# Optimization experiments

Hardware: AMD Instinct MI355X
Metric: run time of the kernel (lower is better)

The kernel has to match this reference:

```python
import jax, jax.numpy as jnp
import numpy as np

L2 = 65536          # edges per orientation (L=256 torus)
N = 2 * L2          # total edges
FIN = 8             # nfeatCNN_in
FOUT = 8            # nfeatCNN_out
K = 13              # kernel size (neighbor shifts per edge)
SCALE = (2.0 + 2.0 * np.e) / (np.e - 1.0)


def setup_inputs() -> dict:
    key = jax.random.key(0)
    ks = jax.random.split(key, 8)
    x = jax.random.normal(ks[0], (FIN * N,), dtype=jnp.float32)
    Wconv_hor = jax.random.normal(ks[1], (FOUT, FIN, K), dtype=jnp.float32) * 0.1
    Wconv_vert = jax.random.normal(ks[2], (FOUT, FIN, K), dtype=jnp.float32) * 0.1
    bconv_hor = jnp.zeros((FOUT,), dtype=jnp.float32)
    bconv_vert = jnp.zeros((FOUT,), dtype=jnp.float32)
    mask_hor = jax.random.randint(ks[3], (L2, FOUT, FIN, K), 0, 2).astype(bool)
    mask_vert = jax.random.randint(ks[4], (L2, FOUT, FIN, K), 0, 2).astype(bool)
    ker_hor = jax.random.randint(ks[5], (L2, K), 0, N, dtype=jnp.int32)
    ker_vert = jax.random.randint(ks[6], (L2, K), 0, N, dtype=jnp.int32)
    hor_edge_lst = jnp.arange(L2, dtype=jnp.int32)
    vert_edge_lst = jnp.arange(L2, dtype=jnp.int32) + L2
    return {
        "x": x,
        "Wconv_hor": Wconv_hor, "Wconv_vert": Wconv_vert,
        "bconv_hor": bconv_hor, "bconv_vert": bconv_vert,
        "mask_hor": mask_hor, "mask_vert": mask_vert,
        "ker_hor": ker_hor, "ker_vert": ker_vert,
        "hor_edge_lst": hor_edge_lst, "vert_edge_lst": vert_edge_lst,
    }


def reference(x, Wconv_hor, Wconv_vert, bconv_hor, bconv_vert,
              mask_hor, mask_vert, ker_hor, ker_vert,
              hor_edge_lst, vert_edge_lst):
    fout, fin, _ = Wconv_hor.shape
    n = x.shape[0] // fin
    xm = x.reshape(fin, n)                      # (fin, N)

    def branch(W, mask, ker, b):
        xg = xm[:, ker]                         # gather -> (fin, E, K)
        Wm = W[None] * mask.astype(W.dtype)     # (E, fout, fin, K)
        # per-edge masked contraction over (fin, K); vectorized over edges
        z = jnp.einsum('eoik,iek->oe', Wm, xg)  # (fout, E)
        return z + b[:, None]

    x_hor = branch(Wconv_hor, mask_hor, ker_hor, bconv_hor)
    x_vert = branch(Wconv_vert, mask_vert, ker_vert, bconv_vert)

    out = jnp.zeros((fout, n), dtype=x.dtype)
    out = out.at[:, hor_edge_lst].set(x_hor)
    out = out.at[:, vert_edge_lst].set(x_vert)
    return (jax.nn.sigmoid(out) - 0.5) * jnp.asarray(SCALE, out.dtype)
```

## Files before the change

kernel.cpp:

```cpp
#include <hip/hip_runtime.h>
#include <math.h>

#define L2C   65536
#define NC    (2 * L2C)
#define FINC  8
#define FOUTC 8
#define KC    13
#define BLOCK 256
#define EPB   4

constexpr double E_D = 2.71828182845904523536;
constexpr float SCALE_F = (float)((2.0 + 2.0 * E_D) / (E_D - 1.0));


__global__ __launch_bounds__(256)
void detect_mask_kernel(const unsigned char* __restrict__ m, int* __restrict__ flag) {
    __shared__ int any_nz;
    if (threadIdx.x == 0) any_nz = 0;
    __syncthreads();
    int local = 0;
    for (int e = threadIdx.x; e < 4096; e += 256) local |= m[(size_t)e * 4 + 1];
    if (local) atomicOr(&any_nz, 1);
    __syncthreads();
    if (threadIdx.x == 0) flag[0] = (any_nz == 0) ? 1 : 0;
}

__global__ __launch_bounds__(256)
void transpose_x_kernel(const float* __restrict__ x, float* __restrict__ xt) {
    int n = blockIdx.x * 256 + threadIdx.x;
    float v[FINC];
#pragma unroll
    for (int i = 0; i < FINC; ++i) v[i] = x[(size_t)i * NC + n];
    float4* dst = reinterpret_cast<float4*>(xt + ((size_t)n << 3));
    dst[0] = make_float4(v[0], v[1], v[2], v[3]);
    dst[1] = make_float4(v[4], v[5], v[6], v[7]);
}

__global__ __launch_bounds__(BLOCK)
void edge_conv_kernel(const float* __restrict__ xt,
                      const int* __restrict__ flag_p,
                      const float* __restrict__ Wh, const float* __restrict__ Wv,
                      const float* __restrict__ bh, const float* __restrict__ bv,
                      const unsigned char* __restrict__ mh,
                      const unsigned char* __restrict__ mv,
                      const int* __restrict__ kh, const int* __restrict__ kv,
                      float* __restrict__ out)
{
    __shared__ float Wsh[FOUTC * FINC * KC];

    const int tid  = threadIdx.x;
    const int lane = tid & 63;
    const int wv_i = tid >> 6;
    const int o    = lane >> 3;
    const int i    = lane & 7;

    const int blk = blockIdx.x;
    const int blocks_per_branch = L2C / EPB;
    const bool hor = (blk < blocks_per_branch);

    const float*         W    = hor ? Wh  : Wv;
    const float*         bias = hor ? bh  : bv;
    const unsigned char* mask = hor ? mh  : mv;
    const int*           ker  = hor ? kh  : kv;
    const int bblk = hor ? blk : blk - blocks_per_branch;
    const int be   = bblk * EPB + wv_i;
    const int col  = hor ? be : (be + L2C);

    const int words = flag_p[0];

    for (int j = tid; j < FOUTC * FINC * KC; j += BLOCK) Wsh[j] = W[j];
    __syncthreads();

    unsigned int mbits;
    if (words) {
        const unsigned int* mw = reinterpret_cast<const unsigned int*>(mask)
                                 + (size_t)be * 832;
        unsigned long long myb = 0;
#pragma unroll
        for (int t = 0; t < 13; ++t) {
            unsigned int w = mw[t * 64 + lane];
            unsigned long long bal = __ballot(w != 0u);
            if (lane == t) myb = bal;
        }
        const int s     = lane * 13;
        const int u0    = s >> 6;
        const int shift = s & 63;
        unsigned long long lo = __shfl(myb, u0);
        unsigned long long hi = __shfl(myb, u0 + 1);
        unsigned int bits = (unsigned int)(lo >> shift);
        if (shift) bits |= (unsigned int)(hi << (64 - shift));
        mbits = bits & 0x1FFFu;
    } else {
        const unsigned char* mrow = mask + (size_t)be * 832 + (size_t)lane * 13;
        unsigned int bits = 0;
#pragma unroll
        for (int k = 0; k < 13; ++k) bits |= (mrow[k] ? 1u : 0u) << k;
        mbits = bits;
    }

    int cols[KC];
#pragma unroll
    for (int k = 0; k < KC; ++k) cols[k] = ker[(size_t)be * KC + k];

    float acc = 0.0f;
#pragma unroll
    for (int k = 0; k < KC; ++k) {
        float xv = xt[((size_t)cols[k] << 3) + i];
        float wk = Wsh[lane * KC + k];
        float wm = (mbits >> k) & 1u ? wk : 0.0f;
        acc = fmaf(wm, xv, acc);
    }

    acc += __shfl_xor(acc, 1);
    acc += __shfl_xor(acc, 2);
    acc += __shfl_xor(acc, 4);

    if (i == 0) {
        float z   = acc + bias[o];
        float sig = 1.0f / (1.0f + __expf(-z));
        out[(size_t)o * NC + col] = (sig - 0.5f) * SCALE_F;
    }
}

extern "C" void kernel_launch(void* const* d_in, const int* in_sizes, int n_in,
                              void* d_out, int out_size, void* d_ws, size_t ws_size,
                              hipStream_t stream) {
    const float*         x   = (const float*)d_in[0];
    const float*         Wh  = (const float*)d_in[1];
    const float*         Wv  = (const float*)d_in[2];
    const float*         bh  = (const float*)d_in[3];
    const float*         bv  = (const float*)d_in[4];
    const unsigned char* mh  = (const unsigned char*)d_in[5];
    const unsigned char* mv  = (const unsigned char*)d_in[6];
    const int*           kh  = (const int*)d_in[7];
    const int*           kv  = (const int*)d_in[8];
    float* out  = (float*)d_out;
    int*   flag = (int*)d_ws;
    float* xt   = (float*)((char*)d_ws + 256);

    detect_mask_kernel<<<1, 256, 0, stream>>>(mh, flag);
    transpose_x_kernel<<<NC / 256, 256, 0, stream>>>(x, xt);
    edge_conv_kernel<<<(2 * L2C) / EPB, BLOCK, 0, stream>>>(
        xt, flag, Wh, Wv, bh, bv, mh, mv, kh, kv, out);
}
```

Measured before the change: 454.7 us.

## Precompute compressed mask bits in separate kernel and shuffle-broadcast gather indices

Adds a pre-pass kernel that turns each edge's mask into 13 ballot-packed 64-bit words in workspace, so the main conv kernel reads 104 bytes per edge instead of scanning the full mask. It also has one lane per k load each index and broadcast it with shuffles, and it hoists the weights into registers. The byte-mask fallback path now uses coalesced ballots. The extra kernel still reads the whole mask once, so total mask traffic is unchanged. The gain depends on better memory-level parallelism and less work in the conv kernel, at the cost of one extra launch and a workspace round trip.

```diff
diff --git a/kernel.cpp b/kernel.cpp
--- a/kernel.cpp
+++ b/kernel.cpp
@@ -12,6 +12,10 @@
 constexpr double E_D = 2.71828182845904523536;
 constexpr float SCALE_F = (float)((2.0 + 2.0 * E_D) / (E_D - 1.0));
 
+#define CMP_OFF   256
+#define CMP_BYTES ((size_t)NC * KC * 8)
+#define XT_OFF    (CMP_OFF + CMP_BYTES)
+#define XT_BYTES  ((size_t)NC * FINC * 4)
 
 __global__ __launch_bounds__(256)
 void detect_mask_kernel(const unsigned char* __restrict__ m, int* __restrict__ flag) {
@@ -37,7 +41,47 @@
 }
 
 __global__ __launch_bounds__(BLOCK)
+void mask_compress_kernel(const int* __restrict__ flag_p,
+                          const unsigned char* __restrict__ mh,
+                          const unsigned char* __restrict__ mv,
+                          unsigned long long* __restrict__ cmp)
+{
+    const int tid  = threadIdx.x;
+    const int lane = tid & 63;
+    const int e    = blockIdx.x * EPB + (tid >> 6);
+    const bool hor = (e < L2C);
+    const unsigned char* mask = hor ? mh : mv;
+    const int be = hor ? e : e - L2C;
+
+    unsigned long long myb = 0;
+    if (flag_p[0]) {
+        const unsigned int* src =
+            reinterpret_cast<const unsigned int*>(mask) + (size_t)be * 832 + lane;
+        unsigned int w[KC];
+#pragma unroll
+        for (int t = 0; t < KC; ++t) w[t] = src[t * 64];
+#pragma unroll
+        for (int t = 0; t < KC; ++t) {
+            unsigned long long bal = __ballot(w[t] != 0u);
+            if (lane == t) myb = bal;
+        }
+    } else {
+        const unsigned char* src = mask + (size_t)be * 832 + lane;
+        unsigned char w[KC];
+#pragma unroll
+        for (int t = 0; t < KC; ++t) w[t] = src[t * 64];
+#pragma unroll
+        for (int t = 0; t < KC; ++t) {
+            unsigned long long bal = __ballot(w[t] != 0);
+            if (lane == t) myb = bal;
+        }
+    }
+    if (lane < KC) cmp[(size_t)e * KC + lane] = myb;
+}
+
+__global__ __launch_bounds__(BLOCK)
 void edge_conv_kernel(const float* __restrict__ xt,
+                      const unsigned long long* __restrict__ cmp, int use_pre,
                       const int* __restrict__ flag_p,
                       const float* __restrict__ Wh, const float* __restrict__ Wv,
                       const float* __restrict__ bh, const float* __restrict__ bv,
@@ -50,7 +94,6 @@
 
     const int tid  = threadIdx.x;
     const int lane = tid & 63;
-    const int wv_i = tid >> 6;
     const int o    = lane >> 3;
     const int i    = lane & 7;
 
@@ -63,51 +106,59 @@
     const unsigned char* mask = hor ? mh  : mv;
     const int*           ker  = hor ? kh  : kv;
     const int bblk = hor ? blk : blk - blocks_per_branch;
-    const int be   = bblk * EPB + wv_i;
+    const int be   = bblk * EPB + (tid >> 6);
     const int col  = hor ? be : (be + L2C);
-
-    const int words = flag_p[0];
+    const int eg   = col;
 
     for (int j = tid; j < FOUTC * FINC * KC; j += BLOCK) Wsh[j] = W[j];
     __syncthreads();
 
-    unsigned int mbits;
-    if (words) {
-        const unsigned int* mw = reinterpret_cast<const unsigned int*>(mask)
-                                 + (size_t)be * 832;
-        unsigned long long myb = 0;
-#pragma unroll
-        for (int t = 0; t < 13; ++t) {
-            unsigned int w = mw[t * 64 + lane];
-            unsigned long long bal = __ballot(w != 0u);
-            if (lane == t) myb = bal;
-        }
-        const int s     = lane * 13;
-        const int u0    = s >> 6;
-        const int shift = s & 63;
-        unsigned long long lo = __shfl(myb, u0);
-        unsigned long long hi = __shfl(myb, u0 + 1);
-        unsigned int bits = (unsigned int)(lo >> shift);
-        if (shift) bits |= (unsigned int)(hi << (64 - shift));
-        mbits = bits & 0x1FFFu;
+    unsigned long long myb = 0;
+    int colv = 0;
+    if (use_pre) {
+        if (lane < KC) {
+            myb  = cmp[(size_t)eg * KC + lane];
+            colv = ker[(size_t)be * KC + lane];
+        }
     } else {
-        const unsigned char* mrow = mask + (size_t)be * 832 + (size_t)lane * 13;
-        unsigned int bits = 0;
-#pragma unroll
-        for (int k = 0; k < 13; ++k) bits |= (mrow[k] ? 1u : 0u) << k;
-        mbits = bits;
-    }
-
-    int cols[KC];
-#pragma unroll
-    for (int k = 0; k < KC; ++k) cols[k] = ker[(size_t)be * KC + k];
+        if (lane < KC) colv = ker[(size_t)be * KC + lane];
+        if (flag_p[0]) {
+            const unsigned int* mw =
+                reinterpret_cast<const unsigned int*>(mask) + (size_t)be * 832 + lane;
+#pragma unroll
+            for (int t = 0; t < KC; ++t) {
+                unsigned long long bal = __ballot(mw[t * 64] != 0u);
+                if (lane == t) myb = bal;
+            }
+        } else {
+            const unsigned char* mb = mask + (size_t)be * 832 + lane;
+#pragma unroll
+            for (int t = 0; t < KC; ++t) {
+                unsigned long long bal = __ballot(mb[t * 64] != 0);
+                if (lane == t) myb = bal;
+            }
+        }
+    }
+
+    const int s     = lane * KC;
+    const int u0    = s >> 6;
+    const int shift = s & 63;
+    unsigned long long lo = __shfl(myb, u0);
+    unsigned long long hi = __shfl(myb, u0 + 1);
+    unsigned int mbits = (unsigned int)(lo >> shift);
+    if (shift) mbits |= (unsigned int)(hi << (64 - shift));
+    mbits &= 0x1FFFu;
+
+    float wreg[KC];
+#pragma unroll
+    for (int k = 0; k < KC; ++k) wreg[k] = Wsh[lane * KC + k];
 
     float acc = 0.0f;
 #pragma unroll
     for (int k = 0; k < KC; ++k) {
-        float xv = xt[((size_t)cols[k] << 3) + i];
-        float wk = Wsh[lane * KC + k];
-        float wm = (mbits >> k) & 1u ? wk : 0.0f;
+        const int c  = __shfl(colv, k);
+        const float xv = xt[((size_t)c << 3) + i];
+        const float wm = ((mbits >> k) & 1u) ? wreg[k] : 0.0f;
         acc = fmaf(wm, xv, acc);
     }
 
@@ -116,8 +167,8 @@
     acc += __shfl_xor(acc, 4);
 
     if (i == 0) {
-        float z   = acc + bias[o];
-        float sig = 1.0f / (1.0f + __expf(-z));
+        const float z   = acc + bias[o];
+        const float sig = 1.0f / (1.0f + __expf(-z));
         out[(size_t)o * NC + col] = (sig - 0.5f) * SCALE_F;
     }
 }
@@ -136,10 +187,17 @@
     const int*           kv  = (const int*)d_in[8];
     float* out  = (float*)d_out;
     int*   flag = (int*)d_ws;
-    float* xt   = (float*)((char*)d_ws + 256);
+
+    const int use_pre = (ws_size >= XT_OFF + XT_BYTES) ? 1 : 0;
+    unsigned long long* cmp = (unsigned long long*)((char*)d_ws + CMP_OFF);
+    float* xt = use_pre ? (float*)((char*)d_ws + XT_OFF)
+                        : (float*)((char*)d_ws + 256);
 
     detect_mask_kernel<<<1, 256, 0, stream>>>(mh, flag);
+    if (use_pre) {
+        mask_compress_kernel<<<NC / EPB, BLOCK, 0, stream>>>(flag, mh, mv, cmp);
+    }
     transpose_x_kernel<<<NC / 256, 256, 0, stream>>>(x, xt);
-    edge_conv_kernel<<<(2 * L2C) / EPB, BLOCK, 0, stream>>>(
-        xt, flag, Wh, Wv, bh, bv, mh, mv, kh, kv, out);
-}
+    edge_conv_kernel<<<NC / EPB, BLOCK, 0, stream>>>(
+        xt, cmp, use_pre, flag, Wh, Wv, bh, bv, mh, mv, kh, kv, out);
+}
```

Result: slower. 507.4 us (+11.6%).

## Process four edges per wavefront with vectorized mask staging through LDS

Applied to the files above, without the earlier changes.

Each wavefront now handles four consecutive edges instead of one. The mask for those edges is loaded with 16-byte vector loads and compacted to bytes in shared memory, the weights are held in registers across edges, and the kernel indices are loaded once and broadcast with shuffles. The aim is fewer, wider memory transactions and less per-edge setup and launch overhead. In exchange it uses more registers and LDS, and its byte-wise LDS reads at stride 13 may cause bank conflicts.

```diff
diff --git a/kernel.cpp b/kernel.cpp
--- a/kernel.cpp
+++ b/kernel.cpp
@@ -7,7 +7,8 @@
 #define FOUTC 8
 #define KC    13
 #define BLOCK 256
-#define EPB   4
+#define EPW   4
+#define EPB   16
 
 constexpr double E_D = 2.71828182845904523536;
 constexpr float SCALE_F = (float)((2.0 + 2.0 * E_D) / (E_D - 1.0));
@@ -47,10 +48,11 @@
                       float* __restrict__ out)
 {
     __shared__ float Wsh[FOUTC * FINC * KC];
+    __shared__ unsigned char nzbuf[4][EPW * 832];
 
     const int tid  = threadIdx.x;
     const int lane = tid & 63;
-    const int wv_i = tid >> 6;
+    const int w    = tid >> 6;
     const int o    = lane >> 3;
     const int i    = lane & 7;
 
@@ -63,62 +65,67 @@
     const unsigned char* mask = hor ? mh  : mv;
     const int*           ker  = hor ? kh  : kv;
     const int bblk = hor ? blk : blk - blocks_per_branch;
-    const int be   = bblk * EPB + wv_i;
-    const int col  = hor ? be : (be + L2C);
+    const int be0  = bblk * EPB + w * EPW;
+    const int c0   = hor ? be0 : be0 + L2C;
 
-    const int words = flag_p[0];
+    int colv = 0;
+    if (lane < EPW * KC) colv = ker[(size_t)be0 * KC + lane];
 
     for (int j = tid; j < FOUTC * FINC * KC; j += BLOCK) Wsh[j] = W[j];
     __syncthreads();
 
-    unsigned int mbits;
-    if (words) {
-        const unsigned int* mw = reinterpret_cast<const unsigned int*>(mask)
-                                 + (size_t)be * 832;
-        unsigned long long myb = 0;
+    float wreg[KC];
 #pragma unroll
-        for (int t = 0; t < 13; ++t) {
-            unsigned int w = mw[t * 64 + lane];
-            unsigned long long bal = __ballot(w != 0u);
-            if (lane == t) myb = bal;
+    for (int k = 0; k < KC; ++k) wreg[k] = Wsh[lane * KC + k];
+
+    unsigned char* nz = &nzbuf[w][0];
+
+    if (flag_p[0]) {
+        const uint4* src = reinterpret_cast<const uint4*>(
+            reinterpret_cast<const unsigned int*>(mask) + (size_t)be0 * 832) + lane;
+        uint4 v[KC];
+#pragma unroll
+        for (int t = 0; t < KC; ++t) v[t] = src[t * 64];
+#pragma unroll
+        for (int t = 0; t < KC; ++t) {
+            unsigned int b4 = (v[t].x ? 0x01u : 0u) | (v[t].y ? 0x0100u : 0u) |
+                              (v[t].z ? 0x010000u : 0u) | (v[t].w ? 0x01000000u : 0u);
+            reinterpret_cast<unsigned int*>(nz)[t * 64 + lane] = b4;
         }
-        const int s     = lane * 13;
-        const int u0    = s >> 6;
-        const int shift = s & 63;
-        unsigned long long lo = __shfl(myb, u0);
-        unsigned long long hi = __shfl(myb, u0 + 1);
-        unsigned int bits = (unsigned int)(lo >> shift);
-        if (shift) bits |= (unsigned int)(hi << (64 - shift));
-        mbits = bits & 0x1FFFu;
     } else {
-        const unsigned char* mrow = mask + (size_t)be * 832 + (size_t)lane * 13;
-        unsigned int bits = 0;
+        const uint4* src = reinterpret_cast<const uint4*>(mask + (size_t)be0 * 832);
 #pragma unroll
-        for (int k = 0; k < 13; ++k) bits |= (mrow[k] ? 1u : 0u) << k;
-        mbits = bits;
+        for (int t = 0; t < 4; ++t) {
+            int idx = t * 64 + lane;
+            if (idx < 208) reinterpret_cast<uint4*>(nz)[idx] = src[idx];
+        }
     }
 
-    int cols[KC];
+    float accs[EPW];
 #pragma unroll
-    for (int k = 0; k < KC; ++k) cols[k] = ker[(size_t)be * KC + k];
-
-    float acc = 0.0f;
+    for (int e = 0; e < EPW; ++e) {
+        float acc = 0.0f;
 #pragma unroll
-    for (int k = 0; k < KC; ++k) {
-        float xv = xt[((size_t)cols[k] << 3) + i];
-        float wk = Wsh[lane * KC + k];
-        float wm = (mbits >> k) & 1u ? wk : 0.0f;
-        acc = fmaf(wm, xv, acc);
+        for (int k = 0; k < KC; ++k) {
+            const int c    = __shfl(colv, e * KC + k);
+            const float xv = xt[((size_t)c << 3) + i];
+            const unsigned char mb = nz[e * 832 + lane * KC + k];
+            acc = fmaf(mb ? wreg[k] : 0.0f, xv, acc);
+        }
+        accs[e] = acc;
     }
 
-    acc += __shfl_xor(acc, 1);
-    acc += __shfl_xor(acc, 2);
-    acc += __shfl_xor(acc, 4);
+#pragma unroll
+    for (int e = 0; e < EPW; ++e) {
+        accs[e] += __shfl_xor(accs[e], 1);
+        accs[e] += __shfl_xor(accs[e], 2);
+        accs[e] += __shfl_xor(accs[e], 4);
+    }
 
-    if (i == 0) {
-        float z   = acc + bias[o];
-        float sig = 1.0f / (1.0f + __expf(-z));
-        out[(size_t)o * NC + col] = (sig - 0.5f) * SCALE_F;
+    if (i < EPW) {
+        const float z   = accs[i] + bias[o];
+        const float sig = 1.0f / (1.0f + __expf(-z));
+        out[(size_t)o * NC + c0 + i] = (sig - 0.5f) * SCALE_F;
     }
 }
 
@@ -140,6 +147,6 @@
 
     detect_mask_kernel<<<1, 256, 0, stream>>>(mh, flag);
     transpose_x_kernel<<<NC / 256, 256, 0, stream>>>(x, xt);
-    edge_conv_kernel<<<(2 * L2C) / EPB, BLOCK, 0, stream>>>(
+    edge_conv_kernel<<<NC / EPB, BLOCK, 0, stream>>>(
         xt, flag, Wh, Wv, bh, bv, mh, mv, kh, kv, out);
 }
```

Result: no change. 453.4 us (-0.3%).
